# Performance work log

Hardware: AMD Instinct MI355X
Metric: run time of the kernel (lower is better)

## Reference

```python
import jax, jax.numpy as jnp
import numpy as np

N_NODES = 50000
N_EDGES = 800000
IN_FEATS = 256
OUT_FEATS = 64
NUM_HEADS = 4
NEG_SLOPE = 0.2


def setup_inputs() -> dict:
    key = jax.random.key(0)
    k1, k2, k3, k4, k5, k6 = jax.random.split(key, 6)
    feat = jax.random.normal(k1, (N_NODES, IN_FEATS), dtype=jnp.float32)
    src = jax.random.randint(k2, (N_EDGES,), 0, N_NODES, dtype=jnp.int32)
    dst = jax.random.randint(k3, (N_EDGES,), 0, N_NODES, dtype=jnp.int32)
    # fc weight (no bias), xavier-like scale
    W = jax.random.normal(k4, (IN_FEATS, NUM_HEADS * OUT_FEATS), dtype=jnp.float32) * 0.05
    attn_l = jax.random.normal(k5, (NUM_HEADS, OUT_FEATS), dtype=jnp.float32) * 0.1
    attn_r = jax.random.normal(k6, (NUM_HEADS, OUT_FEATS), dtype=jnp.float32) * 0.1
    return {"feat": feat, "src": src, "dst": dst, "W": W, "attn_l": attn_l, "attn_r": attn_r}


def reference(feat, src, dst, W, attn_l, attn_r):
    N = feat.shape[0]
    # fc: [N, H*F] -> [N, H, F]
    ft = (feat @ W).reshape(N, NUM_HEADS, OUT_FEATS)
    # per-node attention logits [N, H]
    el = jnp.einsum('nhf,hf->nh', ft, attn_l)
    er = jnp.einsum('nhf,hf->nh', ft, attn_r)
    # edge logits: u_add_v then leaky relu  [E, H]
    e = el[src] + er[dst]
    e = jnp.where(e > 0, e, NEG_SLOPE * e)
    # edge softmax over edges sharing the same dst, numerically stable
    m = jax.ops.segment_max(e, dst, num_segments=N)          # [N, H]
    e_exp = jnp.exp(e - m[dst])                               # [E, H]
    denom = jax.ops.segment_sum(e_exp, dst, num_segments=N)  # [N, H]
    a = e_exp / denom[dst]                                    # [E, H]
    # u_mul_e + sum: gather src features, weight, scatter-add to dst
    msg = ft[src] * a[:, :, None]                             # [E, H, F]
    out = jax.ops.segment_sum(msg, dst, num_segments=N)      # [N, H, F]
    return out
```

## Files before the change

kernel.cpp:

```cpp
#include <hip/hip_runtime.h>
#include <hip/hip_bf16.h>
#include <math.h>

#define N_NODES 50000
#define N_EDGES 800000
#define IN_F 256
#define HF 256
#define NHEAD 4
#define OF 64
#define NPAD 50176
#define CAP 96
#define MPAD 50048
#define GEMM_BLOCKS 782
#define FILL_BLOCKS 1250

typedef __attribute__((ext_vector_type(8))) short short8;
typedef __attribute__((ext_vector_type(4))) float f32x4;

__device__ __forceinline__ ushort f32_to_bf16(float x) {
  unsigned u = __float_as_uint(x);
  u += 0x7FFFu + ((u >> 16) & 1u);
  return (ushort)(u >> 16);
}
__device__ __forceinline__ float bfl(unsigned u) { return __uint_as_float(u << 16); }
__device__ __forceinline__ float bfh(unsigned u) { return __uint_as_float(u & 0xFFFF0000u); }

__device__ __forceinline__ void gload_lds16(const void* g, void* l) {
  __builtin_amdgcn_global_load_lds(
      (const __attribute__((address_space(1))) unsigned int*)g,
      (__attribute__((address_space(3))) unsigned int*)l, 16, 0, 0);
}

__global__ __launch_bounds__(256) void prep(const float* __restrict__ W,
                                            ushort* __restrict__ WT,
                                            int* __restrict__ cnt) {
  int i = blockIdx.x * blockDim.x + threadIdx.x;
  int stride = gridDim.x * blockDim.x;
  for (int j = i; j < IN_F * HF; j += stride) {
    int n = j >> 8, k = j & 255;
    WT[j] = f32_to_bf16(W[k * HF + n]);
  }
  for (int j = i; j < NPAD; j += stride) cnt[j] = 0;
}

__global__ __launch_bounds__(256) void fused_gf(const float* __restrict__ A,
                                                const ushort* __restrict__ BT,
                                                const float* __restrict__ al,
                                                const float* __restrict__ ar,
                                                ushort* __restrict__ C,
                                                float* __restrict__ el,
                                                float* __restrict__ er,
                                                const int* __restrict__ src,
                                                const int* __restrict__ dst,
                                                int* __restrict__ cnt,
                                                int* __restrict__ csr_src) {
  __shared__ char lds[24576];
  int tid = threadIdx.x;

  if (blockIdx.x >= GEMM_BLOCKS) {
    int fb = blockIdx.x - GEMM_BLOCKS;
    int stride = FILL_BLOCKS * 256;
    for (int e = fb * 256 + tid; e < N_EDGES; e += stride) {
      int s = __builtin_nontemporal_load(&src[e]);
      int d = dst[e];
      int p = atomicAdd(&cnt[d], 1);
      if (p < CAP) csr_src[d * CAP + p] = s;
    }
    return;
  }

  char* As = lds;
  char* Bs = lds + 8192;
  int w = tid >> 6, lane = tid & 63;
  int brow = blockIdx.x * 64;
  int rl = lane & 15, khalf = lane >> 4;
  f32x4 acc[4][4];
#pragma unroll
  for (int m = 0; m < 4; ++m)
#pragma unroll
    for (int n = 0; n < 4; ++n) acc[m][n] = (f32x4){0.f, 0.f, 0.f, 0.f};

  for (int k0 = 0; k0 < IN_F; k0 += 32) {
#pragma unroll
    for (int part = 0; part < 2; ++part) {
      int ii = w * 2 + part;
      int d = ii * 1024 + lane * 16;
      int trow = d >> 7;
      int slot = (d >> 4) & 7;
      int srcslot = slot ^ (trow & 7);
      int ga = min(brow + trow, N_NODES - 1);
      gload_lds16(A + (size_t)ga * IN_F + k0 + srcslot * 4, As + d);
    }
#pragma unroll
    for (int part = 0; part < 4; ++part) {
      int ii = w * 4 + part;
      int d = ii * 1024 + lane * 16;
      int trow = d >> 6;
      int slot = (d >> 4) & 3;
      int srcslot = slot ^ ((trow >> 1) & 3);
      gload_lds16(BT + (size_t)trow * IN_F + k0 + srcslot * 8, Bs + d);
    }
    __syncthreads();
    short8 a[4], b[4];
#pragma unroll
    for (int m = 0; m < 4; ++m) {
      int r = m * 16 + rl;
      int s0 = khalf * 2, s1 = khalf * 2 + 1;
      float4 lo = *(const float4*)(As + r * 128 + ((s0 ^ (r & 7)) << 4));
      float4 hi = *(const float4*)(As + r * 128 + ((s1 ^ (r & 7)) << 4));
      union { short8 s; unsigned u[4]; } cv;
      cv.u[0] = __builtin_amdgcn_perm(__float_as_uint(lo.y), __float_as_uint(lo.x), 0x07060302);
      cv.u[1] = __builtin_amdgcn_perm(__float_as_uint(lo.w), __float_as_uint(lo.z), 0x07060302);
      cv.u[2] = __builtin_amdgcn_perm(__float_as_uint(hi.y), __float_as_uint(hi.x), 0x07060302);
      cv.u[3] = __builtin_amdgcn_perm(__float_as_uint(hi.w), __float_as_uint(hi.z), 0x07060302);
      a[m] = cv.s;
    }
#pragma unroll
    for (int n = 0; n < 4; ++n) {
      int c = w * 64 + n * 16 + rl;
      b[n] = *(const short8*)(Bs + c * 64 + ((khalf ^ ((c >> 1) & 3)) << 4));
    }
#pragma unroll
    for (int m = 0; m < 4; ++m)
#pragma unroll
      for (int n = 0; n < 4; ++n)
        acc[m][n] = __builtin_amdgcn_mfma_f32_16x16x32_bf16(a[m], b[n], acc[m][n], 0, 0, 0);
    __syncthreads();
  }

#pragma unroll
  for (int m = 0; m < 4; ++m) {
    int r0 = brow + m * 16 + khalf * 4;
#pragma unroll
    for (int n = 0; n < 4; ++n) {
      int col = w * 64 + n * 16 + rl;
#pragma unroll
      for (int j = 0; j < 4; ++j)
        C[(size_t)(r0 + j) * HF + col] = f32_to_bf16(acc[m][n][j]);
    }
  }

  float alv[4], arv[4];
#pragma unroll
  for (int n = 0; n < 4; ++n) {
    alv[n] = al[w * OF + n * 16 + rl];
    arv[n] = ar[w * OF + n * 16 + rl];
  }
#pragma unroll
  for (int m = 0; m < 4; ++m) {
    int r0 = brow + m * 16 + khalf * 4;
#pragma unroll
    for (int j = 0; j < 4; ++j) {
      float pl = acc[m][0][j] * alv[0] + acc[m][1][j] * alv[1] +
                 acc[m][2][j] * alv[2] + acc[m][3][j] * alv[3];
      float pr = acc[m][0][j] * arv[0] + acc[m][1][j] * arv[1] +
                 acc[m][2][j] * arv[2] + acc[m][3][j] * arv[3];
#pragma unroll
      for (int off2 = 1; off2 < 16; off2 <<= 1) {
        pl += __shfl_xor(pl, off2);
        pr += __shfl_xor(pr, off2);
      }
      int r = r0 + j;
      if (rl == 0 && r < N_NODES) {
        el[r * NHEAD + w] = pl;
        er[r * NHEAD + w] = pr;
      }
    }
  }
}

__global__ __launch_bounds__(256) void aggregate(const int* __restrict__ cnt,
                                                 const int* __restrict__ csr_src,
                                                 const float* __restrict__ el,
                                                 const float* __restrict__ er,
                                                 const ushort* __restrict__ ft,
                                                 float* __restrict__ out) {
  int w = threadIdx.x >> 6, lane = threadIdx.x & 63;
  int n = blockIdx.x * 4 + w;
  if (n >= N_NODES) return;
  int half = lane >> 5, l5 = lane & 31;
  int h = l5 >> 3;
  int c = l5 << 3;
  float erh = er[n * NHEAD + h];
  int j0 = n * CAP;
  int j1 = j0 + min(cnt[n], CAP);
  float a0 = 0.f, a1 = 0.f, a2 = 0.f, a3 = 0.f;
  float a4 = 0.f, a5 = 0.f, a6 = 0.f, a7 = 0.f;
  float den = 0.f;
#pragma unroll 4
  for (int j = j0 + half; j < j1; j += 2) {
    int s = __builtin_nontemporal_load(&csr_src[j]);
    float x = el[s * NHEAD + h] + erh;
    x = x > 0.f ? x : 0.2f * x;
    float a = __expf(x);
    den += a;
    uint4 u = *(const uint4*)(ft + (size_t)s * HF + c);
    a0 += bfl(u.x) * a; a1 += bfh(u.x) * a;
    a2 += bfl(u.y) * a; a3 += bfh(u.y) * a;
    a4 += bfl(u.z) * a; a5 += bfh(u.z) * a;
    a6 += bfl(u.w) * a; a7 += bfh(u.w) * a;
  }
  den += __shfl_xor(den, 32);
  a0 += __shfl_xor(a0, 32); a1 += __shfl_xor(a1, 32);
  a2 += __shfl_xor(a2, 32); a3 += __shfl_xor(a3, 32);
  a4 += __shfl_xor(a4, 32); a5 += __shfl_xor(a5, 32);
  a6 += __shfl_xor(a6, 32); a7 += __shfl_xor(a7, 32);
  if (half == 0) {
    float inv = den > 0.f ? 1.0f / den : 0.f;
    f32x4 r0 = {a0 * inv, a1 * inv, a2 * inv, a3 * inv};
    f32x4 r1 = {a4 * inv, a5 * inv, a6 * inv, a7 * inv};
    __builtin_nontemporal_store(r0, (f32x4*)&out[(size_t)n * HF + c]);
    __builtin_nontemporal_store(r1, (f32x4*)&out[(size_t)n * HF + c + 4]);
  }
}

extern "C" void kernel_launch(void* const* d_in, const int* in_sizes, int n_in,
                              void* d_out, int out_size, void* d_ws, size_t ws_size,
                              hipStream_t stream) {
  const float* feat = (const float*)d_in[0];
  const int*   src  = (const int*)d_in[1];
  const int*   dst  = (const int*)d_in[2];
  const float* W    = (const float*)d_in[3];
  const float* al   = (const float*)d_in[4];
  const float* ar   = (const float*)d_in[5];
  float* out = (float*)d_out;

  char* ws = (char*)d_ws;
  ushort* ft_bf   = (ushort*)(ws);
  int*    csr_src = (int*)(ws + 26000000);
  int*    cnt     = (int*)(ws + 45400000);
  float*  el      = (float*)(ws + 45700000);
  float*  er      = (float*)(ws + 46500000);
  ushort* WT      = (ushort*)(ws + 47300000);

  prep<<<512, 256, 0, stream>>>(W, WT, cnt);
  fused_gf<<<GEMM_BLOCKS + FILL_BLOCKS, 256, 0, stream>>>(feat, WT, al, ar, ft_bf,
                                                          el, er, src, dst, cnt, csr_src);
  aggregate<<<(N_NODES + 3) / 4, 256, 0, stream>>>(cnt, csr_src, el, er, ft_bf, out);
}
```

Before: 150.3 us.

## Interleave GEMM and CSR-fill blocks, double-buffer A tiles, read B from global

Spreads the GEMM blocks evenly among the edge-fill blocks across the grid, so memory-bound atomic fill work and MFMA work run side by side on the compute units instead of in two separate phases. The A tile is double-buffered in LDS, so the next k-slice is prefetched while the current one is consumed. The B operand (the small transposed weight matrix) is now read straight from global memory through the cache instead of being staged in LDS, which cuts LDS use to 16 KB. The trade-off is that uncoalesced global B reads may add latency per MFMA step, and correctness depends on the barriers correctly ordering the asynchronous LDS loads.

```diff
diff --git a/kernel.cpp b/kernel.cpp
--- a/kernel.cpp
+++ b/kernel.cpp
@@ -13,6 +13,7 @@
 #define MPAD 50048
 #define GEMM_BLOCKS 782
 #define FILL_BLOCKS 1250
+#define TOT_BLOCKS (GEMM_BLOCKS + FILL_BLOCKS)
 
 typedef __attribute__((ext_vector_type(8))) short short8;
 typedef __attribute__((ext_vector_type(4))) float f32x4;
@@ -54,11 +55,14 @@
                                                 const int* __restrict__ dst,
                                                 int* __restrict__ cnt,
                                                 int* __restrict__ csr_src) {
-  __shared__ char lds[24576];
+  __shared__ char lds[16384];
   int tid = threadIdx.x;
-
-  if (blockIdx.x >= GEMM_BLOCKS) {
-    int fb = blockIdx.x - GEMM_BLOCKS;
+  int i = blockIdx.x;
+  int g0 = (int)(((long)i * GEMM_BLOCKS) / TOT_BLOCKS);
+  int g1 = (int)(((long)(i + 1) * GEMM_BLOCKS) / TOT_BLOCKS);
+
+  if (g1 == g0) {
+    int fb = i - g0;
     int stride = FILL_BLOCKS * 256;
     for (int e = fb * 256 + tid; e < N_EDGES; e += stride) {
       int s = __builtin_nontemporal_load(&src[e]);
@@ -69,10 +73,10 @@
     return;
   }
 
-  char* As = lds;
-  char* Bs = lds + 8192;
+  char* As0 = lds;
+  char* As1 = lds + 8192;
   int w = tid >> 6, lane = tid & 63;
-  int brow = blockIdx.x * 64;
+  int brow = g0 * 64;
   int rl = lane & 15, khalf = lane >> 4;
   f32x4 acc[4][4];
 #pragma unroll
@@ -80,45 +84,47 @@
 #pragma unroll
     for (int n = 0; n < 4; ++n) acc[m][n] = (f32x4){0.f, 0.f, 0.f, 0.f};
 
-  for (int k0 = 0; k0 < IN_F; k0 += 32) {
-#pragma unroll
-    for (int part = 0; part < 2; ++part) {
-      int ii = w * 2 + part;
-      int d = ii * 1024 + lane * 16;
-      int trow = d >> 7;
-      int slot = (d >> 4) & 7;
-      int srcslot = slot ^ (trow & 7);
-      int ga = min(brow + trow, N_NODES - 1);
-      gload_lds16(A + (size_t)ga * IN_F + k0 + srcslot * 4, As + d);
-    }
-#pragma unroll
-    for (int part = 0; part < 4; ++part) {
-      int ii = w * 4 + part;
-      int d = ii * 1024 + lane * 16;
-      int trow = d >> 6;
-      int slot = (d >> 4) & 3;
-      int srcslot = slot ^ ((trow >> 1) & 3);
-      gload_lds16(BT + (size_t)trow * IN_F + k0 + srcslot * 8, Bs + d);
-    }
-    __syncthreads();
-    short8 a[4], b[4];
+#define STAGE_A(buf, k0)                                                     \
+  {                                                                          \
+    _Pragma("unroll")                                                        \
+    for (int part = 0; part < 2; ++part) {                                   \
+      int ii = w * 2 + part;                                                 \
+      int d = ii * 1024 + lane * 16;                                         \
+      int trow = d >> 7;                                                     \
+      int slot = (d >> 4) & 7;                                               \
+      int srcslot = slot ^ (trow & 7);                                       \
+      int ga = min(brow + trow, N_NODES - 1);                                \
+      gload_lds16(A + (size_t)ga * IN_F + (k0) + srcslot * 4, (buf) + d);    \
+    }                                                                        \
+  }
+
+  STAGE_A(As0, 0);
+  __syncthreads();
+
+  for (int kt = 0; kt < 8; ++kt) {
+    int k0 = kt * 32;
+    char* cur = (kt & 1) ? As1 : As0;
+    char* nxt = (kt & 1) ? As0 : As1;
+    if (kt < 7) STAGE_A(nxt, k0 + 32);
+    short8 b[4];
+#pragma unroll
+    for (int n = 0; n < 4; ++n) {
+      int c = w * 64 + n * 16 + rl;
+      b[n] = *(const short8*)(BT + (size_t)c * IN_F + k0 + khalf * 8);
+    }
+    short8 a[4];
 #pragma unroll
     for (int m = 0; m < 4; ++m) {
       int r = m * 16 + rl;
       int s0 = khalf * 2, s1 = khalf * 2 + 1;
-      float4 lo = *(const float4*)(As + r * 128 + ((s0 ^ (r & 7)) << 4));
-      float4 hi = *(const float4*)(As + r * 128 + ((s1 ^ (r & 7)) << 4));
+      float4 lo = *(const float4*)(cur + r * 128 + ((s0 ^ (r & 7)) << 4));
+      float4 hi = *(const float4*)(cur + r * 128 + ((s1 ^ (r & 7)) << 4));
       union { short8 s; unsigned u[4]; } cv;
       cv.u[0] = __builtin_amdgcn_perm(__float_as_uint(lo.y), __float_as_uint(lo.x), 0x07060302);
       cv.u[1] = __builtin_amdgcn_perm(__float_as_uint(lo.w), __float_as_uint(lo.z), 0x07060302);
       cv.u[2] = __builtin_amdgcn_perm(__float_as_uint(hi.y), __float_as_uint(hi.x), 0x07060302);
       cv.u[3] = __builtin_amdgcn_perm(__float_as_uint(hi.w), __float_as_uint(hi.z), 0x07060302);
       a[m] = cv.s;
-    }
-#pragma unroll
-    for (int n = 0; n < 4; ++n) {
-      int c = w * 64 + n * 16 + rl;
-      b[n] = *(const short8*)(Bs + c * 64 + ((khalf ^ ((c >> 1) & 3)) << 4));
     }
 #pragma unroll
     for (int m = 0; m < 4; ++m)
@@ -234,7 +240,7 @@
   ushort* WT      = (ushort*)(ws + 47300000);
 
   prep<<<512, 256, 0, stream>>>(W, WT, cnt);
-  fused_gf<<<GEMM_BLOCKS + FILL_BLOCKS, 256, 0, stream>>>(feat, WT, al, ar, ft_bf,
-                                                          el, er, src, dst, cnt, csr_src);
+  fused_gf<<<TOT_BLOCKS, 256, 0, stream>>>(feat, WT, al, ar, ft_bf,
+                                           el, er, src, dst, cnt, csr_src);
   aggregate<<<(N_NODES + 3) / 4, 256, 0, stream>>>(cnt, csr_src, el, er, ft_bf, out);
 }
```

Measured after the change: 135.0 us. 10.2% less time.
